# Optimization experiments

Measured on AMD Instinct MI355X. Metric: run time of the kernel, lower is better.

## Reference

```python
import jax, jax.numpy as jnp
import numpy as np

T_OUT = 12  # num_timesteps_output


def setup_inputs() -> dict:
    key = jax.random.key(0)
    ks = jax.random.split(key, 12)
    B, N, T, F = 32, 325, 12, 2
    C, H = 10, 64
    s = 0.08  # weight init scale (~1/sqrt(H)) to keep gates in sane range
    return {
        "A": jnp.zeros((N, N), jnp.float32),
        "X": jax.random.normal(ks[0], (B, N, T, F), jnp.float32),
        "enc_Wih": jax.random.normal(ks[1], (C, 3 * H, F), jnp.float32) * s,
        "enc_Whh": jax.random.normal(ks[2], (C, 3 * H, H), jnp.float32) * s,
        "enc_bih": jax.random.normal(ks[3], (C, 3 * H), jnp.float32) * s,
        "enc_bhh": jax.random.normal(ks[4], (C, 3 * H), jnp.float32) * s,
        "dec_Wih": jax.random.normal(ks[5], (C, 3 * H, 1), jnp.float32) * s,
        "dec_Whh": jax.random.normal(ks[6], (C, 3 * H, H), jnp.float32) * s,
        "dec_bih": jax.random.normal(ks[7], (C, 3 * H), jnp.float32) * s,
        "dec_bhh": jax.random.normal(ks[8], (C, 3 * H), jnp.float32) * s,
        "lin_W": jax.random.normal(ks[9], (C, 1, H), jnp.float32) * s,
        "lin_b": jax.random.normal(ks[10], (C, 1), jnp.float32) * s,
        "embed": jax.random.normal(ks[11], (N, C), jnp.float32),
    }


def _gru_update(gi, gh, h, H):
    # PyTorch GRU gate order: r, z, n
    r = jax.nn.sigmoid(gi[..., :H] + gh[..., :H])
    z = jax.nn.sigmoid(gi[..., H:2 * H] + gh[..., H:2 * H])
    n = jnp.tanh(gi[..., 2 * H:] + r * gh[..., 2 * H:])
    return (1.0 - z) * n + z * h


def reference(A, X, enc_Wih, enc_Whh, enc_bih, enc_bhh,
              dec_Wih, dec_Whh, dec_bih, dec_bhh, lin_W, lin_b, embed):
    B, N, T, F = X.shape
    C = enc_Wih.shape[0]
    H = enc_Whh.shape[-1]
    BN = B * N

    # (T, BN, F): time-major, batch*nodes flattened (matches X.view(-1,T,F).permute(1,0,2))
    Xs = jnp.transpose(X.reshape(BN, T, F), (1, 0, 2))

    def enc_step(h, x_t):  # h: (C, BN, H), x_t: (BN, F)
        gi = jnp.einsum('bf,cgf->cbg', x_t, enc_Wih) + enc_bih[:, None, :]
        gh = jnp.einsum('cbh,cgh->cbg', h, enc_Whh) + enc_bhh[:, None, :]
        return _gru_update(gi, gh, h, H), None

    h0 = jnp.zeros((C, BN, H), X.dtype)
    h_enc, _ = jax.lax.scan(enc_step, h0, Xs)  # (C, BN, H)

    # initial decoder input: last observed value of feature 0
    lv0 = jnp.broadcast_to(Xs[-1, :, 0][None, :, None], (C, BN, 1))

    def dec_step(carry, _):
        h, lv = carry
        gi = jnp.einsum('cbf,cgf->cbg', lv, dec_Wih) + dec_bih[:, None, :]
        gh = jnp.einsum('cbh,cgh->cbg', h, dec_Whh) + dec_bhh[:, None, :]
        h = _gru_update(gi, gh, h, H)
        value = jnp.einsum('cbh,coh->cbo', h, lin_W) + lin_b[:, None, :]  # (C, BN, 1)
        # original does last_value = value.detach()
        return (h, jax.lax.stop_gradient(value)), value

    (_, _), vals = jax.lax.scan(dec_step, (h_enc, lv0), None, length=T_OUT)
    # vals: (T_out, C, BN, 1) -> (B, N, T_out, C)
    out = jnp.transpose(vals[..., 0], (2, 0, 1)).reshape(B, N, T_OUT, C)

    weight = jax.nn.softmax(embed, axis=-1)  # (N, C)
    return jnp.einsum('bntc,nc->bnt', out, weight)
```

## Files before the change

kernel.cpp:

```cpp
#include <hip/hip_runtime.h>
#include <math.h>

#define N_   325
#define BN_  10400
#define R_   32
#define OUTSZ_ (BN_*12)

typedef _Float16 h8v __attribute__((ext_vector_type(8)));
typedef float    f4v __attribute__((ext_vector_type(4)));

#define L1C  1.4426950408889634f
#define L2C  2.8853900817779268f

__device__ __forceinline__ float rcp_f(float x){ return __builtin_amdgcn_rcpf(x); }
#if __has_builtin(__builtin_amdgcn_exp2f)
__device__ __forceinline__ float exp2_f(float x){ return __builtin_amdgcn_exp2f(x); }
#else
__device__ __forceinline__ float exp2_f(float x){ return __expf(x * 0.6931471805599453f); }
#endif

__device__ __forceinline__ int plane_idx(int m,int k){
    return m*64 + ((((k>>3)^(m&7))<<3)|(k&7));
}
__device__ __forceinline__ int frag_idx(int m,int kb){
    return m*64 + ((kb^(m&7))<<3);
}

__device__ __forceinline__ void load_B_scaled(const float* __restrict__ Whh,
                                              int jcol, int kg, h8v Bf[3][2])
{
    const float sc[3] = { -L1C, -L1C, -L2C };
#pragma unroll
    for (int g3=0; g3<3; ++g3)
#pragma unroll
        for (int ch=0; ch<2; ++ch) {
            const float* p = Whh + (g3*64 + jcol)*64 + ch*32 + kg*8;
            float4 a = *(const float4*)p;
            float4 b = *(const float4*)(p+4);
            h8v v;
            v[0]=(_Float16)(sc[g3]*a.x); v[1]=(_Float16)(sc[g3]*a.y);
            v[2]=(_Float16)(sc[g3]*a.z); v[3]=(_Float16)(sc[g3]*a.w);
            v[4]=(_Float16)(sc[g3]*b.x); v[5]=(_Float16)(sc[g3]*b.y);
            v[6]=(_Float16)(sc[g3]*b.z); v[7]=(_Float16)(sc[g3]*b.w);
            Bf[g3][ch] = v;
        }
}

__global__ void __launch_bounds__(256, 4) krnn_kernel(
    const float* __restrict__ X,
    const float* __restrict__ eWih, const float* __restrict__ eWhh,
    const float* __restrict__ ebih, const float* __restrict__ ebhh,
    const float* __restrict__ dWih, const float* __restrict__ dWhh,
    const float* __restrict__ dbih, const float* __restrict__ dbhh,
    const float* __restrict__ linW, const float* __restrict__ linb,
    const float* __restrict__ embed, float* __restrict__ ws)
{
    __shared__ _Float16 sH[2][R_*64];
    __shared__ float2 sX2[12*R_];
    __shared__ float sWgt[R_];

    const int c    = blockIdx.y;
    const int row0 = blockIdx.x * R_;
    const int tid  = threadIdx.x;
    const int lane = tid & 63;
    const int wv   = tid >> 6;
    const int nl   = lane & 15;
    const int kg   = lane >> 4;
    const int jcol = wv*16 + nl;

    for (int i = tid; i < 12*R_; i += 256) {
        int t = i >> 5, m = i & (R_-1);
        const float* p = X + (size_t)(row0+m)*24 + 2*t;
        sX2[i] = make_float2(p[0], p[1]);
    }
    for (int i = tid; i < R_*64; i += 256) sH[1][i] = (_Float16)0.0f;
    if (tid < R_) {
        int n = (row0 + tid) % N_;
        float e[10], mx = -1e30f;
#pragma unroll
        for (int cc=0; cc<10; ++cc){ e[cc]=embed[n*10+cc]; mx=fmaxf(mx,e[cc]); }
        float den = 0.0f;
#pragma unroll
        for (int cc=0; cc<10; ++cc) den += exp2_f((e[cc]-mx)*L1C);
        sWgt[tid] = exp2_f((e[c]-mx)*L1C) * rcp_f(den);
    }

    h8v Bf[3][2];
    load_B_scaled(eWhh + c*12288, jcol, kg, Bf);

    h8v BeR, BeZ, BeN, BeN2;
#pragma unroll
    for (int i=0;i<8;++i){ BeR[i]=(_Float16)0.0f; BeZ[i]=(_Float16)0.0f;
                           BeN[i]=(_Float16)0.0f; BeN2[i]=(_Float16)0.0f; }
    if (kg == 0) {
        int gc = jcol;
        BeR[0]=(_Float16)(-L1C*eWih[c*384 + gc*2]);
        BeR[1]=(_Float16)(-L1C*eWih[c*384 + gc*2 + 1]);
        BeR[2]=(_Float16)(-L1C*(ebih[c*192+gc] + ebhh[c*192+gc]));
        gc = 64 + jcol;
        BeZ[0]=(_Float16)(-L1C*eWih[c*384 + gc*2]);
        BeZ[1]=(_Float16)(-L1C*eWih[c*384 + gc*2 + 1]);
        BeZ[2]=(_Float16)(-L1C*(ebih[c*192+gc] + ebhh[c*192+gc]));
        gc = 128 + jcol;
        BeN[0]=(_Float16)(-L2C*eWih[c*384 + gc*2]);
        BeN[1]=(_Float16)(-L2C*eWih[c*384 + gc*2 + 1]);
        BeN[2]=(_Float16)(-L2C*ebih[c*192+gc]);
        BeN2[2]=(_Float16)(-L2C*ebhh[c*192+gc]);
    }
    h8v Ae[2];
#pragma unroll
    for (int Mt=0;Mt<2;++Mt){
#pragma unroll
        for (int i=0;i<8;++i) Ae[Mt][i]=(_Float16)0.0f;
        if (kg==0) Ae[Mt][2]=(_Float16)1.0f;
    }

    const f4v Z0 = {0.0f,0.0f,0.0f,0.0f};

    float hreg[2][4];
#pragma unroll
    for (int Mt=0;Mt<2;++Mt)
#pragma unroll
        for (int r4=0;r4<4;++r4) hreg[Mt][r4]=0.0f;

    __syncthreads();

    for (int t = 0; t < 12; ++t) {
        const int rp = (t+1)&1, wp = t&1;
        h8v Ah[2][2];
#pragma unroll
        for (int Mt=0; Mt<2; ++Mt)
#pragma unroll
            for (int ch=0; ch<2; ++ch)
                Ah[Mt][ch] = *(const h8v*)&sH[rp][frag_idx(Mt*16+nl, ch*4+kg)];

        if (kg == 0) {
#pragma unroll
            for (int Mt=0; Mt<2; ++Mt) {
                float2 xe = sX2[t*R_ + Mt*16 + nl];
                Ae[Mt][0] = (_Float16)xe.x; Ae[Mt][1] = (_Float16)xe.y;
            }
        }

        f4v a0[2], a1[2], a2[2], a3[2];
#pragma unroll
        for (int Mt=0;Mt<2;++Mt) {
            a0[Mt] = __builtin_amdgcn_mfma_f32_16x16x32_f16(Ae[Mt], BeR,  Z0, 0,0,0);
            a1[Mt] = __builtin_amdgcn_mfma_f32_16x16x32_f16(Ae[Mt], BeZ,  Z0, 0,0,0);
            a2[Mt] = __builtin_amdgcn_mfma_f32_16x16x32_f16(Ae[Mt], BeN2, Z0, 0,0,0);
            a3[Mt] = __builtin_amdgcn_mfma_f32_16x16x32_f16(Ae[Mt], BeN,  Z0, 0,0,0);
#pragma unroll
            for (int ch=0; ch<2; ++ch) {
                a0[Mt] = __builtin_amdgcn_mfma_f32_16x16x32_f16(Ah[Mt][ch], Bf[0][ch], a0[Mt],0,0,0);
                a1[Mt] = __builtin_amdgcn_mfma_f32_16x16x32_f16(Ah[Mt][ch], Bf[1][ch], a1[Mt],0,0,0);
                a2[Mt] = __builtin_amdgcn_mfma_f32_16x16x32_f16(Ah[Mt][ch], Bf[2][ch], a2[Mt],0,0,0);
            }
        }

#pragma unroll
        for (int Mt=0;Mt<2;++Mt)
#pragma unroll
            for (int r4=0;r4<4;++r4) {
                int m = Mt*16 + kg*4 + r4;
                float er = exp2_f(a0[Mt][r4]);
                float rr = rcp_f(1.0f + er);
                float ez = exp2_f(a1[Mt][r4]);
                float en = exp2_f(fmaf(rr, a2[Mt][r4], a3[Mt][r4]));
                float h  = hreg[Mt][r4];
                float aa = 1.0f + ez;
                float den = fmaf(en, aa, aa);
                float t1 = fmaf(-en, ez, ez);
                float t2 = fmaf(en, h, h);
                float hnew = (t1 + t2) * rcp_f(den);
                hreg[Mt][r4] = hnew;
                sH[wp][plane_idx(m,jcol)] = (_Float16)hnew;
            }
        __syncthreads();
    }

    load_B_scaled(dWhh + c*12288, jcol, kg, Bf);
    h8v Blw[2];
#pragma unroll
    for (int ch=0; ch<2; ++ch) {
        const float* p = linW + c*64 + ch*32 + kg*8;
        float4 a = *(const float4*)p;
        float4 b = *(const float4*)(p+4);
        h8v v;
        v[0]=(_Float16)a.x; v[1]=(_Float16)a.y; v[2]=(_Float16)a.z; v[3]=(_Float16)a.w;
        v[4]=(_Float16)b.x; v[5]=(_Float16)b.y; v[6]=(_Float16)b.z; v[7]=(_Float16)b.w;
        Blw[ch] = v;
    }
    float dws0, ks0, dws1, ks1, dwn2, kn, cbh2;
    {
        int gc = jcol;
        dws0 = -L1C*dWih[c*192 + gc];
        ks0  = -L1C*(dbih[c*192 + gc] + dbhh[c*192 + gc]);
        gc = 64 + jcol;
        dws1 = -L1C*dWih[c*192 + gc];
        ks1  = -L1C*(dbih[c*192 + gc] + dbhh[c*192 + gc]);
        gc = 128 + jcol;
        dwn2 = -L2C*dWih[c*192 + gc];
        kn   = -L2C*dbih[c*192 + gc];
        cbh2 = -L2C*dbhh[c*192 + gc];
    }
    const float lb = linb[c];
    float* __restrict__ wsc = ws + (size_t)c * OUTSZ_;

    float lvx[2][4];
#pragma unroll
    for (int Mt=0;Mt<2;++Mt)
#pragma unroll
        for (int r4=0;r4<4;++r4)
            lvx[Mt][r4] = sX2[11*R_ + Mt*16 + kg*4 + r4].x;

    for (int s = 0; s < 12; ++s) {
        const int rp = (s+1)&1, wp = s&1;
        h8v Ah[2][2];
#pragma unroll
        for (int Mt=0; Mt<2; ++Mt)
#pragma unroll
            for (int ch=0; ch<2; ++ch)
                Ah[Mt][ch] = *(const h8v*)&sH[rp][frag_idx(Mt*16+nl, ch*4+kg)];

        f4v a0[2], a1[2], a2[2], av[2];
#pragma unroll
        for (int Mt=0;Mt<2;++Mt) {
            a0[Mt] = __builtin_amdgcn_mfma_f32_16x16x32_f16(Ah[Mt][0], Bf[0][0], Z0, 0,0,0);
            a1[Mt] = __builtin_amdgcn_mfma_f32_16x16x32_f16(Ah[Mt][0], Bf[1][0], Z0, 0,0,0);
            a2[Mt] = __builtin_amdgcn_mfma_f32_16x16x32_f16(Ah[Mt][0], Bf[2][0], Z0, 0,0,0);
            a0[Mt] = __builtin_amdgcn_mfma_f32_16x16x32_f16(Ah[Mt][1], Bf[0][1], a0[Mt],0,0,0);
            a1[Mt] = __builtin_amdgcn_mfma_f32_16x16x32_f16(Ah[Mt][1], Bf[1][1], a1[Mt],0,0,0);
            a2[Mt] = __builtin_amdgcn_mfma_f32_16x16x32_f16(Ah[Mt][1], Bf[2][1], a2[Mt],0,0,0);
        }
        if (s > 0) {
#pragma unroll
            for (int Mt=0;Mt<2;++Mt) {
                av[Mt] = __builtin_amdgcn_mfma_f32_16x16x32_f16(Ah[Mt][0], Blw[0], Z0, 0,0,0);
                av[Mt] = __builtin_amdgcn_mfma_f32_16x16x32_f16(Ah[Mt][1], Blw[1], av[Mt],0,0,0);
            }
        }

#pragma unroll
        for (int Mt=0;Mt<2;++Mt)
#pragma unroll
            for (int r4=0;r4<4;++r4) {
                int m = Mt*16 + kg*4 + r4;
                float lv;
                if (s == 0) lv = lvx[Mt][r4];
                else {
                    lv = av[Mt][r4] + lb;
                    if (wv == 0 && nl == 0)
                        wsc[(size_t)(row0+m)*12 + (s-1)] = sWgt[m]*lv;
                }
                float er = exp2_f(a0[Mt][r4] + fmaf(dws0, lv, ks0));
                float rr = rcp_f(1.0f + er);
                float ez = exp2_f(a1[Mt][r4] + fmaf(dws1, lv, ks1));
                float en = exp2_f(fmaf(rr, a2[Mt][r4] + cbh2, fmaf(dwn2, lv, kn)));
                float h  = hreg[Mt][r4];
                float aa = 1.0f + ez;
                float den = fmaf(en, aa, aa);
                float t1 = fmaf(-en, ez, ez);
                float t2 = fmaf(en, h, h);
                float hnew = (t1 + t2) * rcp_f(den);
                hreg[Mt][r4] = hnew;
                sH[wp][plane_idx(m,jcol)] = (_Float16)hnew;
            }
        __syncthreads();
    }

    {
        f4v av[2];
#pragma unroll
        for (int Mt=0; Mt<2; ++Mt) {
            h8v A0 = *(const h8v*)&sH[1][frag_idx(Mt*16+nl, 0*4+kg)];
            h8v A1 = *(const h8v*)&sH[1][frag_idx(Mt*16+nl, 1*4+kg)];
            av[Mt] = __builtin_amdgcn_mfma_f32_16x16x32_f16(A0, Blw[0], Z0, 0,0,0);
            av[Mt] = __builtin_amdgcn_mfma_f32_16x16x32_f16(A1, Blw[1], av[Mt],0,0,0);
        }
        if (wv == 0 && nl == 0) {
#pragma unroll
            for (int Mt=0;Mt<2;++Mt)
#pragma unroll
                for (int r4=0;r4<4;++r4) {
                    int m = Mt*16 + kg*4 + r4;
                    wsc[(size_t)(row0+m)*12 + 11] = sWgt[m]*(av[Mt][r4] + lb);
                }
        }
    }
}

__global__ void __launch_bounds__(256) mix_kernel(const float* __restrict__ ws,
                                                  float* __restrict__ out)
{
    int i = blockIdx.x * 256 + threadIdx.x;
    if (i < OUTSZ_) {
        float s = 0.0f;
#pragma unroll
        for (int c = 0; c < 10; ++c) s += ws[(size_t)c * OUTSZ_ + i];
        out[i] = s;
    }
}

extern "C" void kernel_launch(void* const* d_in, const int* in_sizes, int n_in,
                              void* d_out, int out_size, void* d_ws, size_t ws_size,
                              hipStream_t stream) {
    const float* X    = (const float*)d_in[1];
    const float* eWih = (const float*)d_in[2];
    const float* eWhh = (const float*)d_in[3];
    const float* ebih = (const float*)d_in[4];
    const float* ebhh = (const float*)d_in[5];
    const float* dWih = (const float*)d_in[6];
    const float* dWhh = (const float*)d_in[7];
    const float* dbih = (const float*)d_in[8];
    const float* dbhh = (const float*)d_in[9];
    const float* linW = (const float*)d_in[10];
    const float* linb = (const float*)d_in[11];
    const float* emb  = (const float*)d_in[12];
    float* ws  = (float*)d_ws;
    float* out = (float*)d_out;

    dim3 grid(BN_ / R_, 10);
    krnn_kernel<<<grid, dim3(256), 0, stream>>>(
        X, eWih, eWhh, ebih, ebhh, dWih, dWhh, dbih, dbhh, linW, linb, emb, ws);
    mix_kernel<<<(OUTSZ_ + 255) / 256, dim3(256), 0, stream>>>(ws, out);
}
```

Baseline: 226.5 us.

## Give each wave its own 16 rows with weights staged in LDS, removing per-step barriers

The work split changes from all four waves sharing 32 rows, each owning 16 hidden columns, to each wave owning 16 independent rows across all 64 hidden columns. Recurrent weights now sit in pre-swizzled LDS fragments instead of registers. Each wave keeps a private h buffer, so the per-timestep __syncthreads disappears and block-wide barriers happen only at the encoder/decoder weight swap. The cost is more LDS traffic per step, since B fragments are re-read from LDS every MFMA, and a 64-row tile that needs bounds clamping for the last block.

```diff
diff --git a/kernel.cpp b/kernel.cpp
--- a/kernel.cpp
+++ b/kernel.cpp
@@ -1,16 +1,17 @@
 #include <hip/hip_runtime.h>
 #include <math.h>
 
-#define N_   325
-#define BN_  10400
-#define R_   32
+#define N_     325
+#define BN_    10400
 #define OUTSZ_ (BN_*12)
 
-typedef _Float16 h8v __attribute__((ext_vector_type(8)));
-typedef float    f4v __attribute__((ext_vector_type(4)));
-
-#define L1C  1.4426950408889634f
-#define L2C  2.8853900817779268f
+
+typedef _Float16 h8v  __attribute__((ext_vector_type(8)));
+typedef float    f4v  __attribute__((ext_vector_type(4)));
+typedef unsigned int u32x4 __attribute__((ext_vector_type(4)));
+
+#define L1C 1.4426950408889634f
+#define L2C 2.8853900817779268f
 
 __device__ __forceinline__ float rcp_f(float x){ return __builtin_amdgcn_rcpf(x); }
 #if __has_builtin(__builtin_amdgcn_exp2f)
@@ -19,31 +20,72 @@
 __device__ __forceinline__ float exp2_f(float x){ return __expf(x * 0.6931471805599453f); }
 #endif
 
-__device__ __forceinline__ int plane_idx(int m,int k){
-    return m*64 + ((((k>>3)^(m&7))<<3)|(k&7));
-}
-__device__ __forceinline__ int frag_idx(int m,int kb){
-    return m*64 + ((kb^(m&7))<<3);
-}
-
-__device__ __forceinline__ void load_B_scaled(const float* __restrict__ Whh,
-                                              int jcol, int kg, h8v Bf[3][2])
-{
-    const float sc[3] = { -L1C, -L1C, -L2C };
-#pragma unroll
-    for (int g3=0; g3<3; ++g3)
-#pragma unroll
-        for (int ch=0; ch<2; ++ch) {
-            const float* p = Whh + (g3*64 + jcol)*64 + ch*32 + kg*8;
-            float4 a = *(const float4*)p;
-            float4 b = *(const float4*)(p+4);
-            h8v v;
-            v[0]=(_Float16)(sc[g3]*a.x); v[1]=(_Float16)(sc[g3]*a.y);
-            v[2]=(_Float16)(sc[g3]*a.z); v[3]=(_Float16)(sc[g3]*a.w);
-            v[4]=(_Float16)(sc[g3]*b.x); v[5]=(_Float16)(sc[g3]*b.y);
-            v[6]=(_Float16)(sc[g3]*b.z); v[7]=(_Float16)(sc[g3]*b.w);
-            Bf[g3][ch] = v;
+__device__ __forceinline__ unsigned short f16u(float x){
+    union { _Float16 h; unsigned short u; } cv; cv.h = (_Float16)x; return cv.u;
+}
+
+#define BOFF   0
+#define EOFF   24576
+#define HOFF   27648
+#define XOFF   36864
+#define LWOFF  36864
+#define WOFF   39936
+#define LOFF   40192
+#define SMEMSZ 40448
+
+#define MFMA(A,B,C) __builtin_amdgcn_mfma_f32_16x16x32_f16((A),(B),(C),0,0,0)
+
+__device__ __forceinline__ void stage_main(const float* __restrict__ W, char* smem, int tid)
+{
+    for (int it = 0; it < 24; ++it) {
+        int q    = (it*256 + tid) * 2;
+        int gc   = q >> 6;
+        int k    = q & 63;
+        int g    = gc >> 6;
+        int colf = gc & 63;
+        int f    = g*8 + (colf >> 4)*2 + (k >> 5);
+        int lanew = ((k >> 3) & 3)*16 + (colf & 15);
+        float sc = (g < 2) ? -L1C : -L2C;
+        float2 wv = *(const float2*)(W + q);
+        unsigned short* d = (unsigned short*)(smem + BOFF + f*1024 + lanew*16 + (k & 7)*2);
+        d[0] = f16u(sc*wv.x);
+        d[1] = f16u(sc*wv.y);
+    }
+}
+
+__device__ __forceinline__ void rnn_step(h8v Aeh, h8v Ah0, h8v Ah1,
+                                         const char* bb, const char* eb,
+                                         const float cbh[4], float (&hreg)[4][4],
+                                         char* wp)
+{
+    const f4v Z0 = {0.f,0.f,0.f,0.f};
+#pragma unroll
+    for (int ct = 0; ct < 4; ++ct) {
+        f4v a0 = MFMA(Aeh, *(const h8v*)(eb + ct*256),       Z0);
+        a0 = MFMA(Ah0, *(const h8v*)(bb + (ct*2   )*1024), a0);
+        a0 = MFMA(Ah1, *(const h8v*)(bb + (ct*2+1 )*1024), a0);
+        f4v a1 = MFMA(Aeh, *(const h8v*)(eb + (4+ct)*256),   Z0);
+        a1 = MFMA(Ah0, *(const h8v*)(bb + (8+ct*2 )*1024), a1);
+        a1 = MFMA(Ah1, *(const h8v*)(bb + (9+ct*2 )*1024), a1);
+        f4v a3 = MFMA(Aeh, *(const h8v*)(eb + (8+ct)*256),   Z0);
+        f4v a2 = MFMA(Ah0, *(const h8v*)(bb + (16+ct*2)*1024), Z0);
+        a2 = MFMA(Ah1, *(const h8v*)(bb + (17+ct*2)*1024), a2);
+#pragma unroll
+        for (int i = 0; i < 4; ++i) {
+            float er = exp2_f(a0[i]);
+            float rr = rcp_f(1.0f + er);
+            float ez = exp2_f(a1[i]);
+            float en = exp2_f(fmaf(rr, a2[i] + cbh[ct], a3[i]));
+            float h  = hreg[ct][i];
+            float aa = 1.0f + ez;
+            float den = fmaf(en, aa, aa);
+            float t1  = fmaf(-en, ez, ez);
+            float t2  = fmaf(en, h, h);
+            float hnew = (t1 + t2) * rcp_f(den);
+            hreg[ct][i] = hnew;
+            *(_Float16*)(wp + i*144 + 32*ct) = (_Float16)hnew;
         }
+    }
 }
 
 __global__ void __launch_bounds__(256, 4) krnn_kernel(
@@ -55,236 +97,152 @@
     const float* __restrict__ linW, const float* __restrict__ linb,
     const float* __restrict__ embed, float* __restrict__ ws)
 {
-    __shared__ _Float16 sH[2][R_*64];
-    __shared__ float2 sX2[12*R_];
-    __shared__ float sWgt[R_];
+    __shared__ __align__(16) char smem[SMEMSZ];
 
     const int c    = blockIdx.y;
-    const int row0 = blockIdx.x * R_;
+    const int row0 = blockIdx.x * 64;
     const int tid  = threadIdx.x;
     const int lane = tid & 63;
-    const int wv   = tid >> 6;
-    const int nl   = lane & 15;
+    const int w    = tid >> 6;
+    const int l15  = lane & 15;
     const int kg   = lane >> 4;
-    const int jcol = wv*16 + nl;
-
-    for (int i = tid; i < 12*R_; i += 256) {
-        int t = i >> 5, m = i & (R_-1);
-        const float* p = X + (size_t)(row0+m)*24 + 2*t;
-        sX2[i] = make_float2(p[0], p[1]);
-    }
-    for (int i = tid; i < R_*64; i += 256) sH[1][i] = (_Float16)0.0f;
-    if (tid < R_) {
-        int n = (row0 + tid) % N_;
+
+    stage_main(eWhh + c*12288, smem, tid);
+
+    if (tid < 192) {
+        int e = tid >> 4, ln = tid & 15;
+        int g = e >> 2, ct = e & 3;
+        int gc = g*64 + ct*16 + ln;
+        float sc = (g < 2) ? -L1C : -L2C;
+        float w0 = eWih[c*384 + gc*2], w1 = eWih[c*384 + gc*2 + 1];
+        float bb_ = (g < 2) ? (ebih[c*192+gc] + ebhh[c*192+gc]) : ebih[c*192+gc];
+        unsigned short* d = (unsigned short*)(smem + EOFF + e*256 + ln*16);
+        d[0] = f16u(sc*w0); d[1] = f16u(sc*w1); d[2] = f16u(sc*bb_);
+        d[3]=0; d[4]=0; d[5]=0; d[6]=0; d[7]=0;
+    }
+    for (int i = tid; i < 768; i += 256) {
+        int r = i / 12, t = i - r*12;
+        int rg = row0 + r; if (rg >= BN_) rg = BN_-1;
+        const float* p = X + (size_t)rg*24 + t*2;
+        unsigned v = (unsigned)f16u(p[0]) | ((unsigned)f16u(p[1]) << 16);
+        *(unsigned*)(smem + XOFF + r*48 + t*4) = v;
+    }
+    if (tid < 64) {
+        int r = row0 + tid; if (r >= BN_) r = BN_-1;
+        int n = r % N_;
         float e[10], mx = -1e30f;
 #pragma unroll
         for (int cc=0; cc<10; ++cc){ e[cc]=embed[n*10+cc]; mx=fmaxf(mx,e[cc]); }
         float den = 0.0f;
 #pragma unroll
         for (int cc=0; cc<10; ++cc) den += exp2_f((e[cc]-mx)*L1C);
-        sWgt[tid] = exp2_f((e[c]-mx)*L1C) * rcp_f(den);
-    }
-
-    h8v Bf[3][2];
-    load_B_scaled(eWhh + c*12288, jcol, kg, Bf);
-
-    h8v BeR, BeZ, BeN, BeN2;
-#pragma unroll
-    for (int i=0;i<8;++i){ BeR[i]=(_Float16)0.0f; BeZ[i]=(_Float16)0.0f;
-                           BeN[i]=(_Float16)0.0f; BeN2[i]=(_Float16)0.0f; }
-    if (kg == 0) {
-        int gc = jcol;
-        BeR[0]=(_Float16)(-L1C*eWih[c*384 + gc*2]);
-        BeR[1]=(_Float16)(-L1C*eWih[c*384 + gc*2 + 1]);
-        BeR[2]=(_Float16)(-L1C*(ebih[c*192+gc] + ebhh[c*192+gc]));
-        gc = 64 + jcol;
-        BeZ[0]=(_Float16)(-L1C*eWih[c*384 + gc*2]);
-        BeZ[1]=(_Float16)(-L1C*eWih[c*384 + gc*2 + 1]);
-        BeZ[2]=(_Float16)(-L1C*(ebih[c*192+gc] + ebhh[c*192+gc]));
-        gc = 128 + jcol;
-        BeN[0]=(_Float16)(-L2C*eWih[c*384 + gc*2]);
-        BeN[1]=(_Float16)(-L2C*eWih[c*384 + gc*2 + 1]);
-        BeN[2]=(_Float16)(-L2C*ebih[c*192+gc]);
-        BeN2[2]=(_Float16)(-L2C*ebhh[c*192+gc]);
-    }
-    h8v Ae[2];
-#pragma unroll
-    for (int Mt=0;Mt<2;++Mt){
-#pragma unroll
-        for (int i=0;i<8;++i) Ae[Mt][i]=(_Float16)0.0f;
-        if (kg==0) Ae[Mt][2]=(_Float16)1.0f;
-    }
-
-    const f4v Z0 = {0.0f,0.0f,0.0f,0.0f};
-
-    float hreg[2][4];
-#pragma unroll
-    for (int Mt=0;Mt<2;++Mt)
-#pragma unroll
-        for (int r4=0;r4<4;++r4) hreg[Mt][r4]=0.0f;
+        *(float*)(smem + WOFF + tid*4) = exp2_f((e[c]-mx)*L1C) * rcp_f(den);
+    }
+    for (int i = tid; i < 2304; i += 256)
+        *(unsigned*)(smem + HOFF + i*4) = 0u;
+
+    float cbh[4];
+#pragma unroll
+    for (int ct=0; ct<4; ++ct) cbh[ct] = -L2C * ebhh[c*192 + 128 + l15 + 16*ct];
 
     __syncthreads();
 
+    float wreg[4];
+#pragma unroll
+    for (int i=0;i<4;++i) wreg[i] = *(const float*)(smem + WOFF + (w*16 + kg*4 + i)*4);
+
+    char* hp = smem + HOFF + w*2304;
+    const int rdo = l15*144 + kg*16;
+    char* wp = hp + kg*576 + l15*2;
+    const char* bb = smem + lane*16;
+    const char* eb = smem + EOFF + l15*16;
+
+    float hreg[4][4];
+#pragma unroll
+    for (int ct=0; ct<4; ++ct)
+#pragma unroll
+        for (int i=0;i<4;++i) hreg[ct][i] = 0.0f;
+
     for (int t = 0; t < 12; ++t) {
-        const int rp = (t+1)&1, wp = t&1;
-        h8v Ah[2][2];
-#pragma unroll
-        for (int Mt=0; Mt<2; ++Mt)
-#pragma unroll
-            for (int ch=0; ch<2; ++ch)
-                Ah[Mt][ch] = *(const h8v*)&sH[rp][frag_idx(Mt*16+nl, ch*4+kg)];
-
-        if (kg == 0) {
-#pragma unroll
-            for (int Mt=0; Mt<2; ++Mt) {
-                float2 xe = sX2[t*R_ + Mt*16 + nl];
-                Ae[Mt][0] = (_Float16)xe.x; Ae[Mt][1] = (_Float16)xe.y;
-            }
-        }
-
-        f4v a0[2], a1[2], a2[2], a3[2];
-#pragma unroll
-        for (int Mt=0;Mt<2;++Mt) {
-            a0[Mt] = __builtin_amdgcn_mfma_f32_16x16x32_f16(Ae[Mt], BeR,  Z0, 0,0,0);
-            a1[Mt] = __builtin_amdgcn_mfma_f32_16x16x32_f16(Ae[Mt], BeZ,  Z0, 0,0,0);
-            a2[Mt] = __builtin_amdgcn_mfma_f32_16x16x32_f16(Ae[Mt], BeN2, Z0, 0,0,0);
-            a3[Mt] = __builtin_amdgcn_mfma_f32_16x16x32_f16(Ae[Mt], BeN,  Z0, 0,0,0);
-#pragma unroll
-            for (int ch=0; ch<2; ++ch) {
-                a0[Mt] = __builtin_amdgcn_mfma_f32_16x16x32_f16(Ah[Mt][ch], Bf[0][ch], a0[Mt],0,0,0);
-                a1[Mt] = __builtin_amdgcn_mfma_f32_16x16x32_f16(Ah[Mt][ch], Bf[1][ch], a1[Mt],0,0,0);
-                a2[Mt] = __builtin_amdgcn_mfma_f32_16x16x32_f16(Ah[Mt][ch], Bf[2][ch], a2[Mt],0,0,0);
-            }
-        }
-
-#pragma unroll
-        for (int Mt=0;Mt<2;++Mt)
-#pragma unroll
-            for (int r4=0;r4<4;++r4) {
-                int m = Mt*16 + kg*4 + r4;
-                float er = exp2_f(a0[Mt][r4]);
-                float rr = rcp_f(1.0f + er);
-                float ez = exp2_f(a1[Mt][r4]);
-                float en = exp2_f(fmaf(rr, a2[Mt][r4], a3[Mt][r4]));
-                float h  = hreg[Mt][r4];
-                float aa = 1.0f + ez;
-                float den = fmaf(en, aa, aa);
-                float t1 = fmaf(-en, ez, ez);
-                float t2 = fmaf(en, h, h);
-                float hnew = (t1 + t2) * rcp_f(den);
-                hreg[Mt][r4] = hnew;
-                sH[wp][plane_idx(m,jcol)] = (_Float16)hnew;
-            }
-        __syncthreads();
-    }
-
-    load_B_scaled(dWhh + c*12288, jcol, kg, Bf);
-    h8v Blw[2];
-#pragma unroll
-    for (int ch=0; ch<2; ++ch) {
-        const float* p = linW + c*64 + ch*32 + kg*8;
-        float4 a = *(const float4*)p;
-        float4 b = *(const float4*)(p+4);
-        h8v v;
-        v[0]=(_Float16)a.x; v[1]=(_Float16)a.y; v[2]=(_Float16)a.z; v[3]=(_Float16)a.w;
-        v[4]=(_Float16)b.x; v[5]=(_Float16)b.y; v[6]=(_Float16)b.z; v[7]=(_Float16)b.w;
-        Blw[ch] = v;
-    }
-    float dws0, ks0, dws1, ks1, dwn2, kn, cbh2;
-    {
-        int gc = jcol;
-        dws0 = -L1C*dWih[c*192 + gc];
-        ks0  = -L1C*(dbih[c*192 + gc] + dbhh[c*192 + gc]);
-        gc = 64 + jcol;
-        dws1 = -L1C*dWih[c*192 + gc];
-        ks1  = -L1C*(dbih[c*192 + gc] + dbhh[c*192 + gc]);
-        gc = 128 + jcol;
-        dwn2 = -L2C*dWih[c*192 + gc];
-        kn   = -L2C*dbih[c*192 + gc];
-        cbh2 = -L2C*dbhh[c*192 + gc];
-    }
+        unsigned xd = *(const unsigned*)(smem + XOFF + (w*16 + l15)*48 + t*4);
+        union { u32x4 u; h8v h; } ae;
+        ae.u.x = (lane < 16) ? xd : 0u;
+        ae.u.y = (lane < 16) ? 0x00003C00u : 0u;
+        ae.u.z = 0u; ae.u.w = 0u;
+        h8v Ah0 = *(const h8v*)(hp + rdo);
+        h8v Ah1 = *(const h8v*)(hp + rdo + 64);
+        rnn_step(ae.h, Ah0, Ah1, bb, eb, cbh, hreg, wp);
+    }
+
+    unsigned aew = (*(const unsigned*)(smem + XOFF + (w*16 + l15)*48 + 44) & 0xFFFFu)
+                   | 0x3C000000u;
+
+    __syncthreads();
+
+    stage_main(dWhh + c*12288, smem, tid);
+    if (tid < 192) {
+        int e = tid >> 4, ln = tid & 15;
+        int g = e >> 2, ct = e & 3;
+        int gc = g*64 + ct*16 + ln;
+        float k0, k1;
+        if (g < 2) { k0 = -L1C*dWih[c*192+gc]; k1 = -L1C*(dbih[c*192+gc]+dbhh[c*192+gc]); }
+        else       { k0 = -L2C*dWih[c*192+gc]; k1 = -L2C*dbih[c*192+gc]; }
+        unsigned short* d = (unsigned short*)(smem + EOFF + e*256 + ln*16);
+        d[0] = f16u(k0); d[1] = f16u(k1);
+        d[2]=0; d[3]=0; d[4]=0; d[5]=0; d[6]=0; d[7]=0;
+    }
+    if (tid < 128) {
+        int ch = tid >> 6, ln = tid & 63;
+        int kb = ch*32 + (ln >> 4)*8;
+        unsigned short* d = (unsigned short*)(smem + LWOFF + ch*1024 + ln*16);
+#pragma unroll
+        for (int j=0;j<8;++j) d[j] = f16u(linW[c*64 + kb + j]);
+    }
+#pragma unroll
+    for (int ct=0; ct<4; ++ct) cbh[ct] = -L2C * dbhh[c*192 + 128 + l15 + 16*ct];
     const float lb = linb[c];
     float* __restrict__ wsc = ws + (size_t)c * OUTSZ_;
 
-    float lvx[2][4];
-#pragma unroll
-    for (int Mt=0;Mt<2;++Mt)
-#pragma unroll
-        for (int r4=0;r4<4;++r4)
-            lvx[Mt][r4] = sX2[11*R_ + Mt*16 + kg*4 + r4].x;
+    __syncthreads();
 
     for (int s = 0; s < 12; ++s) {
-        const int rp = (s+1)&1, wp = s&1;
-        h8v Ah[2][2];
-#pragma unroll
-        for (int Mt=0; Mt<2; ++Mt)
-#pragma unroll
-            for (int ch=0; ch<2; ++ch)
-                Ah[Mt][ch] = *(const h8v*)&sH[rp][frag_idx(Mt*16+nl, ch*4+kg)];
-
-        f4v a0[2], a1[2], a2[2], av[2];
-#pragma unroll
-        for (int Mt=0;Mt<2;++Mt) {
-            a0[Mt] = __builtin_amdgcn_mfma_f32_16x16x32_f16(Ah[Mt][0], Bf[0][0], Z0, 0,0,0);
-            a1[Mt] = __builtin_amdgcn_mfma_f32_16x16x32_f16(Ah[Mt][0], Bf[1][0], Z0, 0,0,0);
-            a2[Mt] = __builtin_amdgcn_mfma_f32_16x16x32_f16(Ah[Mt][0], Bf[2][0], Z0, 0,0,0);
-            a0[Mt] = __builtin_amdgcn_mfma_f32_16x16x32_f16(Ah[Mt][1], Bf[0][1], a0[Mt],0,0,0);
-            a1[Mt] = __builtin_amdgcn_mfma_f32_16x16x32_f16(Ah[Mt][1], Bf[1][1], a1[Mt],0,0,0);
-            a2[Mt] = __builtin_amdgcn_mfma_f32_16x16x32_f16(Ah[Mt][1], Bf[2][1], a2[Mt],0,0,0);
+        h8v Ah0 = *(const h8v*)(hp + rdo);
+        h8v Ah1 = *(const h8v*)(hp + rdo + 64);
+        if (s > 0) {
+            const f4v Zv = {0.f,0.f,0.f,0.f};
+            f4v av = MFMA(Ah0, *(const h8v*)(smem + LWOFF + lane*16), Zv);
+            av = MFMA(Ah1, *(const h8v*)(smem + LWOFF + 1024 + lane*16), av);
+            if (l15 == 0) {
+#pragma unroll
+                for (int i=0;i<4;++i) {
+                    float lv = av[i] + lb;
+                    *(float*)(smem + LOFF + w*64 + (kg*4+i)*4) = lv;
+                    int r = row0 + w*16 + kg*4 + i;
+                    if (r < BN_) wsc[(size_t)r*12 + (s-1)] = wreg[i]*lv;
+                }
+            }
+            float lvme = *(const float*)(smem + LOFF + w*64 + l15*4);
+            aew = (unsigned)f16u(lvme) | 0x3C000000u;
         }
-        if (s > 0) {
-#pragma unroll
-            for (int Mt=0;Mt<2;++Mt) {
-                av[Mt] = __builtin_amdgcn_mfma_f32_16x16x32_f16(Ah[Mt][0], Blw[0], Z0, 0,0,0);
-                av[Mt] = __builtin_amdgcn_mfma_f32_16x16x32_f16(Ah[Mt][1], Blw[1], av[Mt],0,0,0);
+        union { u32x4 u; h8v h; } ae;
+        ae.u.x = (lane < 16) ? aew : 0u;
+        ae.u.y = 0u; ae.u.z = 0u; ae.u.w = 0u;
+        rnn_step(ae.h, Ah0, Ah1, bb, eb, cbh, hreg, wp);
+    }
+
+    {
+        h8v Ah0 = *(const h8v*)(hp + rdo);
+        h8v Ah1 = *(const h8v*)(hp + rdo + 64);
+        const f4v Zv = {0.f,0.f,0.f,0.f};
+        f4v av = MFMA(Ah0, *(const h8v*)(smem + LWOFF + lane*16), Zv);
+        av = MFMA(Ah1, *(const h8v*)(smem + LWOFF + 1024 + lane*16), av);
+        if (l15 == 0) {
+#pragma unroll
+            for (int i=0;i<4;++i) {
+                float lv = av[i] + lb;
+                int r = row0 + w*16 + kg*4 + i;
+                if (r < BN_) wsc[(size_t)r*12 + 11] = wreg[i]*lv;
             }
-        }
-
-#pragma unroll
-        for (int Mt=0;Mt<2;++Mt)
-#pragma unroll
-            for (int r4=0;r4<4;++r4) {
-                int m = Mt*16 + kg*4 + r4;
-                float lv;
-                if (s == 0) lv = lvx[Mt][r4];
-                else {
-                    lv = av[Mt][r4] + lb;
-                    if (wv == 0 && nl == 0)
-                        wsc[(size_t)(row0+m)*12 + (s-1)] = sWgt[m]*lv;
-                }
-                float er = exp2_f(a0[Mt][r4] + fmaf(dws0, lv, ks0));
-                float rr = rcp_f(1.0f + er);
-                float ez = exp2_f(a1[Mt][r4] + fmaf(dws1, lv, ks1));
-                float en = exp2_f(fmaf(rr, a2[Mt][r4] + cbh2, fmaf(dwn2, lv, kn)));
-                float h  = hreg[Mt][r4];
-                float aa = 1.0f + ez;
-                float den = fmaf(en, aa, aa);
-                float t1 = fmaf(-en, ez, ez);
-                float t2 = fmaf(en, h, h);
-                float hnew = (t1 + t2) * rcp_f(den);
-                hreg[Mt][r4] = hnew;
-                sH[wp][plane_idx(m,jcol)] = (_Float16)hnew;
-            }
-        __syncthreads();
-    }
-
-    {
-        f4v av[2];
-#pragma unroll
-        for (int Mt=0; Mt<2; ++Mt) {
-            h8v A0 = *(const h8v*)&sH[1][frag_idx(Mt*16+nl, 0*4+kg)];
-            h8v A1 = *(const h8v*)&sH[1][frag_idx(Mt*16+nl, 1*4+kg)];
-            av[Mt] = __builtin_amdgcn_mfma_f32_16x16x32_f16(A0, Blw[0], Z0, 0,0,0);
-            av[Mt] = __builtin_amdgcn_mfma_f32_16x16x32_f16(A1, Blw[1], av[Mt],0,0,0);
-        }
-        if (wv == 0 && nl == 0) {
-#pragma unroll
-            for (int Mt=0;Mt<2;++Mt)
-#pragma unroll
-                for (int r4=0;r4<4;++r4) {
-                    int m = Mt*16 + kg*4 + r4;
-                    wsc[(size_t)(row0+m)*12 + 11] = sWgt[m]*(av[Mt][r4] + lb);
-                }
         }
     }
 }
@@ -319,7 +277,7 @@
     float* ws  = (float*)d_ws;
     float* out = (float*)d_out;
 
-    dim3 grid(BN_ / R_, 10);
+    dim3 grid((BN_ + 63) / 64, 10);
     krnn_kernel<<<grid, dim3(256), 0, stream>>>(
         X, eWih, eWhh, ebih, ebhh, dWih, dWhh, dbih, dbhh, linW, linb, emb, ws);
     mix_kernel<<<(OUTSZ_ + 255) / 256, dim3(256), 0, stream>>>(ws, out);
```

Measured after the change: 224.5 us. About the same (-0.9%).
